# Kernel optimization log

Hardware: AMD Instinct MI355X
Metric: run time of the kernel (lower is better)

Reference implementation:

```python
import jax, jax.numpy as jnp
import numpy as np

N = 100000      # nodes
DEG = 16        # in-degree per node
E = N * DEG     # edges
IN_DIM = 128
OUT_DIM = 32
EPS = 1e-8      # torch cosine_similarity norm clamp


def setup_inputs() -> dict:
    key = jax.random.key(0)
    k1, k2, k3, k4 = jax.random.split(key, 4)
    h = jax.random.normal(k1, (N, IN_DIM), dtype=jnp.float32)
    # xavier_uniform-scaled linear weight, shape [out_dim, in_dim] like nn.Linear
    W = jax.random.normal(k2, (OUT_DIM, IN_DIM), dtype=jnp.float32) * (1.0 / np.sqrt(IN_DIM))
    beta = jax.random.uniform(k3, (1,), dtype=jnp.float32)
    src = jax.random.randint(k4, (E,), 0, N)
    dst = jnp.arange(E) // DEG  # each node gets exactly DEG incoming edges
    return {"h": h, "W": W, "beta": beta, "src": src, "dst": dst}


def reference(h, W, beta, src, dst):
    # Note: F.dropout(p=0.6) from the original is omitted for a deterministic reference.
    z = h @ W.T                                   # [N, out_dim]
    zs = z[src]                                   # [E, out_dim] gather src features
    zd = z[dst]                                   # [E, out_dim] gather dst features
    num = jnp.sum(zs * zd, axis=-1)               # [E]
    ns = jnp.maximum(jnp.linalg.norm(zs, axis=-1), EPS)
    nd = jnp.maximum(jnp.linalg.norm(zd, axis=-1), EPS)
    cos = num / (ns * nd)                         # torch.cosine_similarity
    e = -beta[0] * (1.0 - cos)                    # [E] edge score
    # segment softmax over incoming edges of each dst node (stable)
    m = jax.ops.segment_max(e, dst, num_segments=N)
    m = jnp.where(jnp.isfinite(m), m, 0.0)        # guard isolated nodes
    ex = jnp.exp(e - m[dst])                      # [E]
    denom = jax.ops.segment_sum(ex, dst, num_segments=N)
    alpha = ex / denom[dst]                       # [E] attention weights
    # weighted scatter-sum of src features to dst nodes
    return jax.ops.segment_sum(alpha[:, None] * zs, dst, num_segments=N)  # [N, out_dim]
```

## Files before the change

kernel.cpp:

```cpp
#include <hip/hip_runtime.h>

#define IN_DIM 128
#define OUT_DIM 32
#define DEG 16
#define EPS 1e-8f

typedef __attribute__((ext_vector_type(8))) short bf16x8;
typedef __attribute__((ext_vector_type(4))) float f32x4;

#define SWZ(x, p) __int_as_float(__builtin_amdgcn_ds_swizzle(__float_as_int(x), (p)))

static __device__ __forceinline__ unsigned short f2bf(float x) {
  unsigned u = __float_as_uint(x);
  u += 0x7FFFu + ((u >> 16) & 1u);
  return (unsigned short)(u >> 16);
}
static __device__ __forceinline__ float bflo(unsigned u) { return __uint_as_float(u << 16); }
static __device__ __forceinline__ float bfhi(unsigned u) { return __uint_as_float(u & 0xFFFF0000u); }

static __device__ __forceinline__ bf16x8 pack8(float4 a, float4 b) {
  bf16x8 r;
  r[0] = (short)f2bf(a.x); r[1] = (short)f2bf(a.y);
  r[2] = (short)f2bf(a.z); r[3] = (short)f2bf(a.w);
  r[4] = (short)f2bf(b.x); r[5] = (short)f2bf(b.y);
  r[6] = (short)f2bf(b.z); r[7] = (short)f2bf(b.w);
  return r;
}

__global__ __launch_bounds__(256) void gemm_norm_kernel(
    const float* __restrict__ h, const float* __restrict__ W,
    unsigned short* __restrict__ zhb, float* __restrict__ invn, int N) {
  __shared__ float pss[2][32];

  const int tid = threadIdx.x;
  const int wv = tid >> 6;
  const int l = tid & 63;
  const int n16 = l & 15;
  const int q = l >> 4;
  const int ng = wv >> 1, oh = wv & 1;
  const int mb = blockIdx.x * 32 + ng * 16;

  bf16x8 bfr[4];
  {
    const float* wr = W + (size_t)(oh * 16 + n16) * IN_DIM + q * 8;
#pragma unroll
    for (int c = 0; c < 4; ++c) {
      const float4 w0 = *(const float4*)(wr + c * 32);
      const float4 w1 = *(const float4*)(wr + c * 32 + 4);
      bfr[c] = pack8(w0, w1);
    }
  }
  int m = mb + n16;
  if (m >= N) m = N - 1;
  bf16x8 afr[4];
  {
    const float* hr = h + (size_t)m * IN_DIM + q * 8;
#pragma unroll
    for (int c = 0; c < 4; ++c) {
      const float4 a0 = *(const float4*)(hr + c * 32);
      const float4 a1 = *(const float4*)(hr + c * 32 + 4);
      afr[c] = pack8(a0, a1);
    }
  }

  f32x4 acc = {0.f, 0.f, 0.f, 0.f};
#pragma unroll
  for (int c = 0; c < 4; ++c)
    acc = __builtin_amdgcn_mfma_f32_16x16x32_bf16(afr[c], bfr[c], acc, 0, 0, 0);

  float sq[4];
#pragma unroll
  for (int r = 0; r < 4; ++r) {
    float s = acc[r] * acc[r];
    s += SWZ(s, 0x041F);
    s += SWZ(s, 0x081F);
    s += SWZ(s, 0x101F);
    s += SWZ(s, 0x201F);
    sq[r] = s;
  }
  if (n16 == 0) {
#pragma unroll
    for (int r = 0; r < 4; ++r) pss[oh][ng * 16 + q * 4 + r] = sq[r];
  }

#pragma unroll
  for (int r = 0; r < 4; ++r) {
    const float partner = SWZ(acc[r], 0x041F);
    const int node = mb + q * 4 + r;
    if (((n16 & 1) == 0) && node < N) {
      const unsigned pk = (unsigned)f2bf(acc[r]) | ((unsigned)f2bf(partner) << 16);
      *(unsigned*)(zhb + (size_t)node * OUT_DIM + oh * 16 + n16) = pk;
    }
  }

  __syncthreads();
  if (tid < 32) {
    const int node = blockIdx.x * 32 + tid;
    const float ss = pss[0][tid] + pss[1][tid];
    if (node < N) invn[node] = 1.0f / fmaxf(sqrtf(ss), EPS);
  }
}

__global__ __launch_bounds__(256) void edge_kernel(
    const unsigned short* __restrict__ zhb, const float* __restrict__ invn,
    const int* __restrict__ src, const float* __restrict__ beta_p,
    float* __restrict__ out, int N) {
  __shared__ float xp[16 * DEG * 36];

  const int tid = threadIdx.x;
  const int l5 = tid & 31, half = (tid >> 5) & 1, wv = tid >> 6;
  const int e = l5 >> 1, c = l5 & 1;
  const int base = (blockIdx.x * 4 + wv) * 4;
  if (base >= N) return;
  const float beta = *beta_p;

  int n_[2], ne_[2];
#pragma unroll
  for (int p = 0; p < 2; ++p) {
    n_[p] = base + p * 2 + half;
    ne_[p] = (n_[p] < N) ? n_[p] : N - 1;
  }

  int se_[2]; float is_[2], id_[2];
  uint4 sa_[2], sb_[2], da_[2], db_[2];
#pragma unroll
  for (int p = 0; p < 2; ++p) {
    se_[p] = src[(size_t)ne_[p] * DEG + e];
    is_[p] = invn[se_[p]];
    id_[p] = invn[ne_[p]];
    const uint4* zs4 = (const uint4*)(zhb + (size_t)se_[p] * OUT_DIM) + c * 2;
    sa_[p] = zs4[0]; sb_[p] = zs4[1];
    const uint4* zd4 = (const uint4*)(zhb + (size_t)ne_[p] * OUT_DIM) + c * 2;
    da_[p] = zd4[0]; db_[p] = zd4[1];
  }

#pragma unroll
  for (int p = 0; p < 2; ++p) {
    float vs[16], vd[16];
    const uint4 sa = sa_[p], sb = sb_[p], da = da_[p], db = db_[p];
    vs[0] = bflo(sa.x);  vs[1] = bfhi(sa.x);  vs[2] = bflo(sa.y);  vs[3] = bfhi(sa.y);
    vs[4] = bflo(sa.z);  vs[5] = bfhi(sa.z);  vs[6] = bflo(sa.w);  vs[7] = bfhi(sa.w);
    vs[8] = bflo(sb.x);  vs[9] = bfhi(sb.x);  vs[10] = bflo(sb.y); vs[11] = bfhi(sb.y);
    vs[12] = bflo(sb.z); vs[13] = bfhi(sb.z); vs[14] = bflo(sb.w); vs[15] = bfhi(sb.w);
    vd[0] = bflo(da.x);  vd[1] = bfhi(da.x);  vd[2] = bflo(da.y);  vd[3] = bfhi(da.y);
    vd[4] = bflo(da.z);  vd[5] = bfhi(da.z);  vd[6] = bflo(da.w);  vd[7] = bfhi(da.w);
    vd[8] = bflo(db.x);  vd[9] = bfhi(db.x);  vd[10] = bflo(db.y); vd[11] = bfhi(db.y);
    vd[12] = bflo(db.z); vd[13] = bfhi(db.z); vd[14] = bflo(db.w); vd[15] = bfhi(db.w);

    float pr = vs[0] * vd[0];
#pragma unroll
    for (int i = 1; i < 16; ++i) pr = fmaf(vs[i], vd[i], pr);
    pr += SWZ(pr, 0x041F);

    const float cosv = pr * is_[p] * id_[p];
    const float ex = __expf(beta * (cosv - 1.0f));

    float den = ex;
    den += SWZ(den, 0x081F);
    den += SWZ(den, 0x101F);
    den += SWZ(den, 0x201F);
    den += SWZ(den, 0x401F);
    const float rd = 1.0f / den;

    float* slot = xp + ((wv * 2 + p) * 2 + half) * (DEG * 36);
    float4* wp = (float4*)(slot + e * 36 + c * 16);
    wp[0] = make_float4(ex * vs[0], ex * vs[1], ex * vs[2], ex * vs[3]);
    wp[1] = make_float4(ex * vs[4], ex * vs[5], ex * vs[6], ex * vs[7]);
    wp[2] = make_float4(ex * vs[8], ex * vs[9], ex * vs[10], ex * vs[11]);
    wp[3] = make_float4(ex * vs[12], ex * vs[13], ex * vs[14], ex * vs[15]);

    float s = 0.f;
#pragma unroll
    for (int e2 = 0; e2 < DEG; ++e2)
      s += slot[e2 * 36 + l5];

    if (n_[p] < N) out[(size_t)n_[p] * OUT_DIM + l5] = s * rd;
  }
}

extern "C" void kernel_launch(void* const* d_in, const int* in_sizes, int n_in,
                              void* d_out, int out_size, void* d_ws, size_t ws_size,
                              hipStream_t stream) {
  const float* h    = (const float*)d_in[0];
  const float* W    = (const float*)d_in[1];
  const float* beta = (const float*)d_in[2];
  const int*   src  = (const int*)d_in[3];

  const int N = in_sizes[0] / IN_DIM;

  unsigned short* zhb = (unsigned short*)d_ws;
  float* invn = (float*)(zhb + (size_t)N * OUT_DIM);

  const int bl1 = (N + 31) / 32;
  gemm_norm_kernel<<<bl1, 256, 0, stream>>>(h, W, zhb, invn, N);

  const int bl2 = (N + 15) / 16;
  edge_kernel<<<bl2, 256, 0, stream>>>(zhb, invn, src, beta, (float*)d_out, N);
}
```

Measured before the change: 137.0 us.

## Store normalized z in bf16 and process one node pair per wave

The GEMM kernel now normalizes z by its L2 norm before the bf16 store and writes the raw norm instead of the inverse norm. The edge kernel computes the cosine directly as a dot product of normalized vectors and rescales the source features by the source norm when aggregating, which removes the destination-norm load. Each wave now handles two nodes instead of four, so the grid doubles and LDS per block halves, giving more parallelism but less per-thread memory-level parallelism. Cosines and features now both pass through bf16 rounding of normalized values, which slightly changes the numerics.

```diff
diff --git a/kernel.cpp b/kernel.cpp
--- a/kernel.cpp
+++ b/kernel.cpp
@@ -29,7 +29,7 @@
 
 __global__ __launch_bounds__(256) void gemm_norm_kernel(
     const float* __restrict__ h, const float* __restrict__ W,
-    unsigned short* __restrict__ zhb, float* __restrict__ invn, int N) {
+    unsigned short* __restrict__ zhb, float* __restrict__ nrm, int N) {
   __shared__ float pss[2][32];
 
   const int tid = threadIdx.x;
@@ -68,7 +68,6 @@
   for (int c = 0; c < 4; ++c)
     acc = __builtin_amdgcn_mfma_f32_16x16x32_bf16(afr[c], bfr[c], acc, 0, 0, 0);
 
-  float sq[4];
 #pragma unroll
   for (int r = 0; r < 4; ++r) {
     float s = acc[r] * acc[r];
@@ -76,106 +75,91 @@
     s += SWZ(s, 0x081F);
     s += SWZ(s, 0x101F);
     s += SWZ(s, 0x201F);
-    sq[r] = s;
+    if (n16 == 0) pss[oh][ng * 16 + q * 4 + r] = s;
   }
-  if (n16 == 0) {
-#pragma unroll
-    for (int r = 0; r < 4; ++r) pss[oh][ng * 16 + q * 4 + r] = sq[r];
-  }
+  __syncthreads();
 
 #pragma unroll
   for (int r = 0; r < 4; ++r) {
-    const float partner = SWZ(acc[r], 0x041F);
+    const int idx = ng * 16 + q * 4 + r;
+    const float ss = pss[0][idx] + pss[1][idx];
+    const float inv = 1.0f / fmaxf(sqrtf(ss), EPS);
+    const float zn = acc[r] * inv;
+    const float partner = SWZ(zn, 0x041F);
     const int node = mb + q * 4 + r;
     if (((n16 & 1) == 0) && node < N) {
-      const unsigned pk = (unsigned)f2bf(acc[r]) | ((unsigned)f2bf(partner) << 16);
+      const unsigned pk = (unsigned)f2bf(zn) | ((unsigned)f2bf(partner) << 16);
       *(unsigned*)(zhb + (size_t)node * OUT_DIM + oh * 16 + n16) = pk;
     }
   }
-
-  __syncthreads();
   if (tid < 32) {
     const int node = blockIdx.x * 32 + tid;
-    const float ss = pss[0][tid] + pss[1][tid];
-    if (node < N) invn[node] = 1.0f / fmaxf(sqrtf(ss), EPS);
+    if (node < N) nrm[node] = sqrtf(pss[0][tid] + pss[1][tid]);
   }
 }
 
 __global__ __launch_bounds__(256) void edge_kernel(
-    const unsigned short* __restrict__ zhb, const float* __restrict__ invn,
+    const unsigned short* __restrict__ zhb, const float* __restrict__ nrm,
     const int* __restrict__ src, const float* __restrict__ beta_p,
     float* __restrict__ out, int N) {
-  __shared__ float xp[16 * DEG * 36];
+  __shared__ float xp[8 * DEG * 36];
 
   const int tid = threadIdx.x;
   const int l5 = tid & 31, half = (tid >> 5) & 1, wv = tid >> 6;
+  const int gw = blockIdx.x * 4 + wv;
+  if (gw * 2 >= N) return;
+  const int n = gw * 2 + half;
+  const int ne = (n < N) ? n : N - 1;
   const int e = l5 >> 1, c = l5 & 1;
-  const int base = (blockIdx.x * 4 + wv) * 4;
-  if (base >= N) return;
+
   const float beta = *beta_p;
+  const int se = src[(size_t)ne * DEG + e];
+  const float nrm_s = nrm[se];
 
-  int n_[2], ne_[2];
+  const uint4* zs4 = (const uint4*)(zhb + (size_t)se * OUT_DIM) + c * 2;
+  const uint4 sa = zs4[0], sb = zs4[1];
+  const uint4* zd4 = (const uint4*)(zhb + (size_t)ne * OUT_DIM) + c * 2;
+  const uint4 da = zd4[0], db = zd4[1];
+
+  float vs[16];
+  vs[0] = bflo(sa.x);  vs[1] = bfhi(sa.x);  vs[2] = bflo(sa.y);  vs[3] = bfhi(sa.y);
+  vs[4] = bflo(sa.z);  vs[5] = bfhi(sa.z);  vs[6] = bflo(sa.w);  vs[7] = bfhi(sa.w);
+  vs[8] = bflo(sb.x);  vs[9] = bfhi(sb.x);  vs[10] = bflo(sb.y); vs[11] = bfhi(sb.y);
+  vs[12] = bflo(sb.z); vs[13] = bfhi(sb.z); vs[14] = bflo(sb.w); vs[15] = bfhi(sb.w);
+  float vd[16];
+  vd[0] = bflo(da.x);  vd[1] = bfhi(da.x);  vd[2] = bflo(da.y);  vd[3] = bfhi(da.y);
+  vd[4] = bflo(da.z);  vd[5] = bfhi(da.z);  vd[6] = bflo(da.w);  vd[7] = bfhi(da.w);
+  vd[8] = bflo(db.x);  vd[9] = bfhi(db.x);  vd[10] = bflo(db.y); vd[11] = bfhi(db.y);
+  vd[12] = bflo(db.z); vd[13] = bfhi(db.z); vd[14] = bflo(db.w); vd[15] = bfhi(db.w);
+
+  float pr = vs[0] * vd[0];
 #pragma unroll
-  for (int p = 0; p < 2; ++p) {
-    n_[p] = base + p * 2 + half;
-    ne_[p] = (n_[p] < N) ? n_[p] : N - 1;
-  }
+  for (int i = 1; i < 16; ++i) pr = fmaf(vs[i], vd[i], pr);
+  pr += SWZ(pr, 0x041F);
 
-  int se_[2]; float is_[2], id_[2];
-  uint4 sa_[2], sb_[2], da_[2], db_[2];
+  const float ex = __expf(beta * (pr - 1.0f));
+
+  float den = ex;
+  den += SWZ(den, 0x081F);
+  den += SWZ(den, 0x101F);
+  den += SWZ(den, 0x201F);
+  den += SWZ(den, 0x401F);
+  const float rd = 1.0f / den;
+
+  const float sc = ex * nrm_s;
+  float* slot = xp + (wv * 2 + half) * (DEG * 36);
+  float4* wp = (float4*)(slot + e * 36 + c * 16);
+  wp[0] = make_float4(sc * vs[0], sc * vs[1], sc * vs[2], sc * vs[3]);
+  wp[1] = make_float4(sc * vs[4], sc * vs[5], sc * vs[6], sc * vs[7]);
+  wp[2] = make_float4(sc * vs[8], sc * vs[9], sc * vs[10], sc * vs[11]);
+  wp[3] = make_float4(sc * vs[12], sc * vs[13], sc * vs[14], sc * vs[15]);
+
+  float s = 0.f;
 #pragma unroll
-  for (int p = 0; p < 2; ++p) {
-    se_[p] = src[(size_t)ne_[p] * DEG + e];
-    is_[p] = invn[se_[p]];
-    id_[p] = invn[ne_[p]];
-    const uint4* zs4 = (const uint4*)(zhb + (size_t)se_[p] * OUT_DIM) + c * 2;
-    sa_[p] = zs4[0]; sb_[p] = zs4[1];
-    const uint4* zd4 = (const uint4*)(zhb + (size_t)ne_[p] * OUT_DIM) + c * 2;
-    da_[p] = zd4[0]; db_[p] = zd4[1];
-  }
+  for (int e2 = 0; e2 < DEG; ++e2)
+    s += slot[e2 * 36 + l5];
 
-#pragma unroll
-  for (int p = 0; p < 2; ++p) {
-    float vs[16], vd[16];
-    const uint4 sa = sa_[p], sb = sb_[p], da = da_[p], db = db_[p];
-    vs[0] = bflo(sa.x);  vs[1] = bfhi(sa.x);  vs[2] = bflo(sa.y);  vs[3] = bfhi(sa.y);
-    vs[4] = bflo(sa.z);  vs[5] = bfhi(sa.z);  vs[6] = bflo(sa.w);  vs[7] = bfhi(sa.w);
-    vs[8] = bflo(sb.x);  vs[9] = bfhi(sb.x);  vs[10] = bflo(sb.y); vs[11] = bfhi(sb.y);
-    vs[12] = bflo(sb.z); vs[13] = bfhi(sb.z); vs[14] = bflo(sb.w); vs[15] = bfhi(sb.w);
-    vd[0] = bflo(da.x);  vd[1] = bfhi(da.x);  vd[2] = bflo(da.y);  vd[3] = bfhi(da.y);
-    vd[4] = bflo(da.z);  vd[5] = bfhi(da.z);  vd[6] = bflo(da.w);  vd[7] = bfhi(da.w);
-    vd[8] = bflo(db.x);  vd[9] = bfhi(db.x);  vd[10] = bflo(db.y); vd[11] = bfhi(db.y);
-    vd[12] = bflo(db.z); vd[13] = bfhi(db.z); vd[14] = bflo(db.w); vd[15] = bfhi(db.w);
-
-    float pr = vs[0] * vd[0];
-#pragma unroll
-    for (int i = 1; i < 16; ++i) pr = fmaf(vs[i], vd[i], pr);
-    pr += SWZ(pr, 0x041F);
-
-    const float cosv = pr * is_[p] * id_[p];
-    const float ex = __expf(beta * (cosv - 1.0f));
-
-    float den = ex;
-    den += SWZ(den, 0x081F);
-    den += SWZ(den, 0x101F);
-    den += SWZ(den, 0x201F);
-    den += SWZ(den, 0x401F);
-    const float rd = 1.0f / den;
-
-    float* slot = xp + ((wv * 2 + p) * 2 + half) * (DEG * 36);
-    float4* wp = (float4*)(slot + e * 36 + c * 16);
-    wp[0] = make_float4(ex * vs[0], ex * vs[1], ex * vs[2], ex * vs[3]);
-    wp[1] = make_float4(ex * vs[4], ex * vs[5], ex * vs[6], ex * vs[7]);
-    wp[2] = make_float4(ex * vs[8], ex * vs[9], ex * vs[10], ex * vs[11]);
-    wp[3] = make_float4(ex * vs[12], ex * vs[13], ex * vs[14], ex * vs[15]);
-
-    float s = 0.f;
-#pragma unroll
-    for (int e2 = 0; e2 < DEG; ++e2)
-      s += slot[e2 * 36 + l5];
-
-    if (n_[p] < N) out[(size_t)n_[p] * OUT_DIM + l5] = s * rd;
-  }
+  if (n < N) out[(size_t)n * OUT_DIM + l5] = s * rd;
 }
 
 extern "C" void kernel_launch(void* const* d_in, const int* in_sizes, int n_in,
@@ -189,11 +173,11 @@
   const int N = in_sizes[0] / IN_DIM;
 
   unsigned short* zhb = (unsigned short*)d_ws;
-  float* invn = (float*)(zhb + (size_t)N * OUT_DIM);
+  float* nrm = (float*)(zhb + (size_t)N * OUT_DIM);
 
   const int bl1 = (N + 31) / 32;
-  gemm_norm_kernel<<<bl1, 256, 0, stream>>>(h, W, zhb, invn, N);
+  gemm_norm_kernel<<<bl1, 256, 0, stream>>>(h, W, zhb, nrm, N);
 
-  const int bl2 = (N + 15) / 16;
-  edge_kernel<<<bl2, 256, 0, stream>>>(zhb, invn, src, beta, (float*)d_out, N);
+  const int bl2 = (N + 7) / 8;
+  edge_kernel<<<bl2, 256, 0, stream>>>(zhb, nrm, src, beta, (float*)d_out, N);
 }
```

Measured after the change: 137.4 us. No clear change (+0.3%).
